# Performance work log

Measured on AMD Instinct MI355X. Metric: run time of the kernel, lower is better.

The kernel has to match this reference:

```python
import jax, jax.numpy as jnp
import numpy as np

V, E, U, B, S = 32000, 512, 1024, 16, 128
BN_EPS = 1e-3  # keras BatchNormalization default


def setup_inputs() -> dict:
    key = jax.random.key(0)
    ks = jax.random.split(key, 12)
    w = 0.05  # small init keeps the relu-activated LSTM recurrence stable
    return {
        "inputs": jax.random.randint(ks[0], (B, S), 0, V),
        "enc_hidden": jax.random.normal(ks[1], (B, U), jnp.float32) * 0.1,
        "enc_cell": jax.random.normal(ks[2], (B, U), jnp.float32) * 0.1,
        "emb": jax.random.normal(ks[3], (V, E), jnp.float32) * w,
        "Wx": jax.random.normal(ks[4], (E, 4 * U), jnp.float32) * w,
        "Wh": jax.random.normal(ks[5], (U, 4 * U), jnp.float32) * w,
        "b": jnp.zeros((4 * U,), jnp.float32),
        "gamma": jnp.ones((U,), jnp.float32),
        "beta": jnp.zeros((U,), jnp.float32),
        "mov_mean": jnp.zeros((U,), jnp.float32),
        "mov_var": jnp.ones((U,), jnp.float32),
        "W1": jax.random.normal(ks[6], (U, U), jnp.float32) * w,
        "b1": jnp.zeros((U,), jnp.float32),
        "W2": jax.random.normal(ks[7], (U, V), jnp.float32) * w,
        "b2": jnp.zeros((V,), jnp.float32),
    }


def _lstm_relu(xg, mask, h0, c0, Wh):
    # xg: [S,B,4U] precomputed input gates; mask: [S,B] (mask_zero semantics)
    def step(carry, inp):
        h, c = carry
        g, m = inp
        z = g + h @ Wh  # [B,4U]
        i, f, cc, o = jnp.split(z, 4, axis=-1)  # keras gate order i,f,c,o
        i = jax.nn.sigmoid(i)
        f = jax.nn.sigmoid(f)
        o = jax.nn.sigmoid(o)
        cc = jax.nn.relu(cc)  # activation='relu' on candidate
        c_new = f * c + i * cc
        h_new = o * jax.nn.relu(c_new)  # activation='relu' on output
        m = m[:, None]
        h_new = jnp.where(m, h_new, h)  # masked step: carry state/output
        c_new = jnp.where(m, c_new, c)
        return (h_new, c_new), h_new

    (_, _), hs = jax.lax.scan(step, (h0, c0), (xg, mask))
    return hs  # [S,B,U]


def reference(inputs, enc_hidden, enc_cell, emb, Wx, Wh, b, gamma, beta,
              mov_mean, mov_var, W1, b1, W2, b2):
    x = emb[inputs]                       # [B,S,E]
    mask = (inputs != 0)                  # mask_zero=True
    xg = jnp.einsum("bse,eg->bsg", x, Wx) + b   # [B,S,4U]
    hs = _lstm_relu(xg.transpose(1, 0, 2), mask.T, enc_hidden, enc_cell, Wh)
    h = hs.transpose(1, 0, 2)             # [B,S,U]
    # BatchNorm (inference: moving statistics), Dropout is identity at inference
    hbn = (h - mov_mean) * jax.lax.rsqrt(mov_var + BN_EPS) * gamma + beta
    d1 = jax.nn.relu(hbn @ W1 + b1)       # [B,S,U]
    logits = d1 @ W2 + b2                 # [B,S,V]
    return jax.nn.softmax(logits, axis=-1)
```

## Files before the change

kernel.cpp:

```cpp
#include <hip/hip_runtime.h>
#include <hip/hip_bf16.h>
#include <stdint.h>

typedef unsigned short u16;
typedef unsigned int u32;
typedef unsigned long long u64;
typedef __attribute__((ext_vector_type(4))) float f32x4;
typedef __attribute__((ext_vector_type(8))) short s16x8;
typedef __attribute__((ext_vector_type(4))) unsigned int u32x4;

#define AT_LD(p)    __hip_atomic_load((p), __ATOMIC_RELAXED, __HIP_MEMORY_SCOPE_AGENT)
#define AT_ST(p, v) __hip_atomic_store((p), (v), __ATOMIC_RELAXED, __HIP_MEMORY_SCOPE_AGENT)
#define AT_FAA(p)   __hip_atomic_fetch_add((p), 1u, __ATOMIC_RELAXED, __HIP_MEMORY_SCOPE_AGENT)


static __device__ __forceinline__ u16 f2bf(float f) {
  union { float f; unsigned u; } v; v.f = f;
  unsigned r = v.u + 0x7FFFu + ((v.u >> 16) & 1u);
  return (u16)(r >> 16);
}

static __device__ __forceinline__ float bf2f(u16 b) {
  union { unsigned u; float f; } v; v.u = ((u32)b) << 16;
  return v.f;
}

static __device__ __forceinline__ void gload_lds16(const void* g, void* l) {
  __builtin_amdgcn_global_load_lds(
      (const __attribute__((address_space(1))) unsigned int*)(uintptr_t)g,
      (__attribute__((address_space(3))) unsigned int*)(uintptr_t)l,
      16, 0, 0);
}

static __device__ __forceinline__ int swzB(int B) {
  int pos = (B >> 4) & 127;
  int row = (B >> 11) & 15;
  int slot = (pos ^ row ^ (pos >> 3)) & 7;
  int npos = (pos & 0x78) | slot;
  return (B & ~0x7F0) | (npos << 4);
}


__global__ void embed_kernel(const int* __restrict__ inputs,
                             const float* __restrict__ emb,
                             u16* __restrict__ xbf) {
  int i = blockIdx.x * 256 + threadIdx.x;
  int row = i >> 6;
  int e0 = (i & 63) << 3;
  int tok = inputs[row];
  const float* src = emb + (size_t)tok * 512 + e0;
  s16x8 o;
#pragma unroll
  for (int j = 0; j < 8; ++j) o[j] = (short)f2bf(src[j]);
  *(s16x8*)(xbf + (size_t)row * 512 + e0) = o;
}

__global__ void mask_kernel(const int* __restrict__ inputs, u64* __restrict__ mb) {
  int t = threadIdx.x;
  if (t < 32) {
    int b = t >> 1, h = t & 1;
    u64 m = 0;
    for (int j = 0; j < 64; ++j)
      m |= (u64)(inputs[b * 128 + h * 64 + j] != 0) << j;
    mb[t] = m;
  }
}

__global__ void transpose_bf16(const float* __restrict__ W, u16* __restrict__ Wt,
                               int K, int N) {
  __shared__ float t[32][33];
  int ntn = N >> 5;
  int tn = blockIdx.x % ntn, tk = blockIdx.x / ntn;
  int n0 = tn << 5, k0 = tk << 5;
  int tx = threadIdx.x & 31, ty = threadIdx.x >> 5;
#pragma unroll
  for (int j = 0; j < 4; ++j) {
    int k = ty * 4 + j;
    t[k][tx] = W[(size_t)(k0 + k) * N + n0 + tx];
  }
  __syncthreads();
#pragma unroll
  for (int j = 0; j < 4; ++j) {
    int n = ty * 4 + j;
    Wt[(size_t)(n0 + n) * K + k0 + tx] = f2bf(t[tx][n]);
  }
}

template <int MODE>
__global__ __launch_bounds__(256)
void gemm_bf16(const u16* __restrict__ A, const u16* __restrict__ Bt,
               const float* __restrict__ bias, void* __restrict__ Cptr,
               float* __restrict__ rowsum, int M, int N, int K) {
  (void)M;
  __shared__ u16 sA[128 * 32];
  __shared__ u16 sB[128 * 32];
  const int nbn = N >> 7;
  const int nwg = gridDim.x;
  int bid = blockIdx.x;
  int q = nwg >> 3;
  int swz = (bid & 7) * q + (bid >> 3);
  int bm = swz / nbn, bn = swz % nbn;
  const int brow = bm << 7, bcol = bn << 7;

  const int tid = threadIdx.x;
  const int lane = tid & 63;
  const int wv = tid >> 6;
  const int wr = (wv >> 1) * 64, wc = (wv & 1) * 64;
  const int ln = lane & 15, kh = lane >> 4;

  const int srow = tid >> 2;
  const int kch = (tid & 3) << 3;

  f32x4 acc[4][4] = {};

  const int nk = K >> 5;
  const u16* Abase = A + (size_t)(brow + srow) * K + kch;
  const u16* Bbase = Bt + (size_t)(bcol + srow) * K + kch;
  const size_t rstride = (size_t)64 * K;
  u16* lA = sA + srow * 32 + kch;
  u16* lB = sB + srow * 32 + kch;

  for (int kt = 0; kt < nk; ++kt) {
    const int k0 = kt << 5;
    gload_lds16(Abase + k0, lA);
    gload_lds16(Abase + rstride + k0, lA + 64 * 32);
    gload_lds16(Bbase + k0, lB);
    gload_lds16(Bbase + rstride + k0, lB + 64 * 32);
    __syncthreads();
    s16x8 aF[4], bF[4];
#pragma unroll
    for (int m = 0; m < 4; ++m)
      aF[m] = *(const s16x8*)(sA + (wr + m * 16 + ln) * 32 + kh * 8);
#pragma unroll
    for (int n = 0; n < 4; ++n)
      bF[n] = *(const s16x8*)(sB + (wc + n * 16 + ln) * 32 + kh * 8);
#pragma unroll
    for (int m = 0; m < 4; ++m)
#pragma unroll
      for (int n = 0; n < 4; ++n)
        acc[m][n] = __builtin_amdgcn_mfma_f32_16x16x32_bf16(aF[m], bF[n], acc[m][n], 0, 0, 0);
    __syncthreads();
  }

  const int browq = brow + wr;
  const int bcolq = bcol + wc;

  if (MODE == 1) {
    u16* O = (u16*)Cptr;
#pragma unroll
    for (int n = 0; n < 4; ++n) {
      int gcol = bcolq + n * 16 + ln;
      float bv = bias[gcol];
#pragma unroll
      for (int m = 0; m < 4; ++m)
#pragma unroll
        for (int r = 0; r < 4; ++r) {
          int grow = browq + m * 16 + kh * 4 + r;
          float v = fmaxf(acc[m][n][r] + bv, 0.f);
          O[(size_t)grow * N + gcol] = f2bf(v);
        }
    }
  } else {
    float* O = (float*)Cptr;
    float rs[4][4] = {};
#pragma unroll
    for (int n = 0; n < 4; ++n) {
      int gcol = bcolq + n * 16 + ln;
      float bv = bias[gcol];
#pragma unroll
      for (int m = 0; m < 4; ++m)
#pragma unroll
        for (int r = 0; r < 4; ++r) {
          int grow = browq + m * 16 + kh * 4 + r;
          float v = acc[m][n][r] + bv;
          if (MODE == 2) { v = __expf(v); rs[m][r] += v; }
          O[(size_t)grow * N + gcol] = v;
        }
    }
    if (MODE == 2) {
#pragma unroll
      for (int m = 0; m < 4; ++m)
#pragma unroll
        for (int r = 0; r < 4; ++r) {
          float v = rs[m][r];
          v += __shfl_xor(v, 1);
          v += __shfl_xor(v, 2);
          v += __shfl_xor(v, 4);
          v += __shfl_xor(v, 8);
          if (ln == 0) atomicAdd(&rowsum[browq + m * 16 + kh * 4 + r], v);
        }
    }
  }
}

__global__ __launch_bounds__(512, 1)
void gemm256_exp(const u16* __restrict__ A, const u16* __restrict__ Bt,
                 const float* __restrict__ bias, u16* __restrict__ O,
                 float* __restrict__ rowsum, int M, int N, int K) {
  (void)M;
  __shared__ char lds[131072];
  const int nbn = N >> 8;
  const int nwg = gridDim.x;
  int bid = blockIdx.x;
  int q = nwg >> 3;
  int swz = (bid & 7) * q + (bid >> 3);
  int bm = swz / nbn, bn = swz % nbn;
  const int brow = bm << 8, bcol = bn << 8;

  const int tid = threadIdx.x;
  const int lane = tid & 63;
  const int wv = tid >> 6;
  const int wm = wv >> 2, wn = wv & 3;
  const int ln = lane & 15, kh = lane >> 4;

  const int nk = K >> 5;

  const u16* sbase[4];
#pragma unroll
  for (int j = 0; j < 4; ++j) {
    int cc = (j & 1) * 512 + wv * 64 + lane;
    int row = cc >> 2, pcol = cc & 3;
    int lcol = pcol ^ ((row >> 1) & 3);
    sbase[j] = (j < 2 ? A + (size_t)(brow + row) * K
                      : Bt + (size_t)(bcol + row) * K) + lcol * 8;
  }

#define STAGE256(kt, buf)                                                  \
  {                                                                        \
    char* lb = lds + (buf) * 32768 + wv * 1024;                            \
    _Pragma("unroll")                                                      \
    for (int j = 0; j < 4; ++j)                                            \
      gload_lds16(sbase[j] + (kt) * 32, lb + j * 8192);                    \
  }

  f32x4 acc[8][4] = {};

  STAGE256(0, 0);
  STAGE256(1, 1);
  asm volatile("s_waitcnt vmcnt(4)" ::: "memory");
  __syncthreads();

  const char* Ab = lds + (size_t)(wm * 128) * 64;
  const char* Bb = lds + 16384 + (size_t)(wn * 64) * 64;
  const int cswz = (kh ^ ((ln >> 1) & 3)) * 16 + ln * 64;

  for (int t = 0; t < nk; ++t) {
    const int boff = (t & 3) * 32768;
    if (t + 2 < nk) STAGE256(t + 2, (t + 2) & 3);
    s16x8 aF[8], bF[4];
#pragma unroll
    for (int m = 0; m < 8; ++m)
      aF[m] = *(const s16x8*)(Ab + boff + m * 1024 + cswz);
#pragma unroll
    for (int n = 0; n < 4; ++n)
      bF[n] = *(const s16x8*)(Bb + boff + n * 1024 + cswz);
    __builtin_amdgcn_s_setprio(1);
#pragma unroll
    for (int m = 0; m < 8; ++m)
#pragma unroll
      for (int n = 0; n < 4; ++n)
        acc[m][n] = __builtin_amdgcn_mfma_f32_16x16x32_bf16(aF[m], bF[n], acc[m][n], 0, 0, 0);
    __builtin_amdgcn_s_setprio(0);
    if (t + 2 < nk)
      asm volatile("s_waitcnt vmcnt(4)" ::: "memory");
    else
      asm volatile("s_waitcnt vmcnt(0)" ::: "memory");
    if (t < nk - 1) __syncthreads();
  }

  const int browq = brow + wm * 128;
  const int bcolq = bcol + wn * 64;
  float rs[8][4] = {};
#pragma unroll
  for (int n = 0; n < 4; ++n) {
    int gcol = bcolq + n * 16 + ln;
    float bv = bias[gcol];
#pragma unroll
    for (int m = 0; m < 8; ++m)
#pragma unroll
      for (int r = 0; r < 4; ++r) {
        float v = __expf(acc[m][n][r] + bv);
        rs[m][r] += v;
        O[(size_t)(browq + m * 16 + kh * 4 + r) * N + gcol] = f2bf(v);
      }
  }
#pragma unroll
  for (int m = 0; m < 8; ++m)
#pragma unroll
    for (int r = 0; r < 4; ++r) {
      float v = rs[m][r];
      v += __shfl_xor(v, 1);
      v += __shfl_xor(v, 2);
      v += __shfl_xor(v, 4);
      v += __shfl_xor(v, 8);
      if (ln == 0) atomicAdd(&rowsum[browq + m * 16 + kh * 4 + r], v);
    }
#undef STAGE256
}

__global__ __attribute__((amdgpu_flat_work_group_size(512, 512), amdgpu_waves_per_eu(2, 2)))
void lstm_kernel(const float* __restrict__ xg,
                 const u16* __restrict__ Wht,
                 const u64* __restrict__ maskb,
                 const float* __restrict__ ench, const float* __restrict__ encc,
                 const float* __restrict__ gamma, const float* __restrict__ beta,
                 const float* __restrict__ mmean, const float* __restrict__ mvar,
                 u32* __restrict__ hbuf32,
                 u16* __restrict__ hbn,
                 u32* __restrict__ cnt) {
  __shared__ char hA[32 * 1024];

  const int wg = blockIdx.x;
  const int u0 = wg << 5;
  const int tid = threadIdx.x;
  const int lane = tid & 63;
  const int wv = tid >> 6;
  const int ln = lane & 15, khq = lane >> 4;

  const int g = ln & 3;
  const int unit = u0 + wv * 4 + (ln >> 2);

  u32 bA[128];
  {
    const u16* wrow = Wht + (size_t)(g * 1024 + unit) * 1024 + khq * 8;
#pragma unroll
    for (int gq = 0; gq < 4; ++gq) {
      u32x4 t[8];
#pragma unroll
      for (int j = 0; j < 8; ++j) {
        const u16* pp = wrow + (gq * 8 + j) * 32;
        asm volatile("global_load_dwordx4 %0, %1, off" : "=v"(t[j]) : "v"(pp));
      }
      asm volatile("s_waitcnt vmcnt(0)" ::: "memory");
      __builtin_amdgcn_sched_barrier(0);
#pragma unroll
      for (int j = 0; j < 8; ++j) {
        int base = (gq * 8 + j) * 4;
        asm volatile("v_accvgpr_write_b32 %0, %1" : "=a"(bA[base + 0]) : "v"(t[j].x));
        asm volatile("v_accvgpr_write_b32 %0, %1" : "=a"(bA[base + 1]) : "v"(t[j].y));
        asm volatile("v_accvgpr_write_b32 %0, %1" : "=a"(bA[base + 2]) : "v"(t[j].z));
        asm volatile("v_accvgpr_write_b32 %0, %1" : "=a"(bA[base + 3]) : "v"(t[j].w));
      }
    }
  }

  float cellR[4], holdR[4], xgr[4];
  u64 mA[4], mB[4];
  const float bn_s = gamma[unit] * rsqrtf(mvar[unit] + 1e-3f);
  const float bn_b = beta[unit] - mmean[unit] * bn_s;
  const size_t bstride = (size_t)128 * 4096;
  const float* xbase = xg + (size_t)(khq * 4) * bstride + g * 1024 + unit;
#pragma unroll
  for (int r = 0; r < 4; ++r) {
    int batch = khq * 4 + r;
    cellR[r] = encc[batch * 1024 + unit];
    holdR[r] = ench[batch * 1024 + unit];
    mA[r] = maskb[batch * 2];
    mB[r] = maskb[batch * 2 + 1];
  }
#pragma unroll
  for (int r = 0; r < 4; ++r) {
    u32 w = (u32)f2bf(holdR[r]);
    u32 pw = (u32)__shfl_xor((int)w, 4);
    if ((ln & 7) == 0) {
      int batch = khq * 4 + r;
      AT_ST((u32*)((char*)hbuf32 + batch * 2048 + unit * 2), (w & 0xFFFFu) | (pw << 16));
    }
  }
#pragma unroll
  for (int r = 0; r < 4; ++r) xgr[r] = xbase[r * bstride];
  asm volatile("s_waitcnt vmcnt(0)" ::: "memory");
  __syncthreads();
  if (tid == 0) {
    u32 oldv = AT_FAA(cnt);
    if (oldv != 31u) {
      int c = 0;
      while (AT_LD((const u32*)cnt) < 32u) {
        __builtin_amdgcn_s_sleep(1);
        if (++c > (1 << 18)) break;
      }
    }
  }
  __syncthreads();

  for (int s = 0; s < 128; ++s) {
    u64 st[8];
    {
      const u64* base = (const u64*)((const char*)hbuf32 + (s & 1) * 32768) + tid;
#pragma unroll
      for (int k = 0; k < 8; ++k) {
        const u64* pp = base + k * 512;
        asm volatile("global_load_dwordx2 %0, %1, off sc0 sc1" : "=v"(st[k]) : "v"(pp));
      }
      asm volatile("s_waitcnt vmcnt(0)" ::: "memory");
      __builtin_amdgcn_sched_barrier(0);
#pragma unroll
      for (int k = 0; k < 8; ++k)
        *(u64*)(hA + swzB((tid + k * 512) * 8)) = st[k];
    }
    __syncthreads();

    f32x4 acc0 = {0.f, 0.f, 0.f, 0.f};
    f32x4 acc1 = {0.f, 0.f, 0.f, 0.f};
#pragma unroll
    for (int kt = 0; kt < 32; kt += 2) {
      s16x8 a0 = *(const s16x8*)(hA + swzB(ln * 2048 + kt * 64 + khq * 16));
      u32 w0, w1, w2, w3;
      asm("v_accvgpr_read_b32 %0, %1" : "=v"(w0) : "a"(bA[4 * kt + 0]));
      asm("v_accvgpr_read_b32 %0, %1" : "=v"(w1) : "a"(bA[4 * kt + 1]));
      asm("v_accvgpr_read_b32 %0, %1" : "=v"(w2) : "a"(bA[4 * kt + 2]));
      asm("v_accvgpr_read_b32 %0, %1" : "=v"(w3) : "a"(bA[4 * kt + 3]));
      u32x4 q0 = {w0, w1, w2, w3};
      acc0 = __builtin_amdgcn_mfma_f32_16x16x32_bf16(
          a0, __builtin_bit_cast(s16x8, q0), acc0, 0, 0, 0);
      s16x8 a1 = *(const s16x8*)(hA + swzB(ln * 2048 + (kt + 1) * 64 + khq * 16));
      u32 y0, y1, y2, y3;
      asm("v_accvgpr_read_b32 %0, %1" : "=v"(y0) : "a"(bA[4 * kt + 4]));
      asm("v_accvgpr_read_b32 %0, %1" : "=v"(y1) : "a"(bA[4 * kt + 5]));
      asm("v_accvgpr_read_b32 %0, %1" : "=v"(y2) : "a"(bA[4 * kt + 6]));
      asm("v_accvgpr_read_b32 %0, %1" : "=v"(y3) : "a"(bA[4 * kt + 7]));
      u32x4 q1 = {y0, y1, y2, y3};
      acc1 = __builtin_amdgcn_mfma_f32_16x16x32_bf16(
          a1, __builtin_bit_cast(s16x8, q1), acc1, 0, 0, 0);
    }
    f32x4 accs = acc0 + acc1;

    u32 bnpair[4];
    {
      u16 hbb[4], hbnb[4];
#pragma unroll
      for (int r = 0; r < 4; ++r) {
        float z = accs[r] + xgr[r];
        float sig = 1.f / (1.f + __expf(-z));
        float val = (g == 2) ? fmaxf(z, 0.f) : sig;
        float v1 = __shfl_xor(val, 1);
        float v2 = __shfl_xor(val, 2);
        float v3 = __shfl_xor(val, 3);
        float cnew = v1 * cellR[r] + val * v2;
        float hnew = v3 * fmaxf(cnew, 0.f);
        u64 mm = (s < 64) ? mA[r] : mB[r];
        if (!((mm >> (s & 63)) & 1)) { cnew = cellR[r]; hnew = holdR[r]; }
        cellR[r] = cnew;
        holdR[r] = hnew;
        hbb[r] = f2bf(hnew);
        hbnb[r] = f2bf(hnew * bn_s + bn_b);
      }
#pragma unroll
      for (int r = 0; r < 4; ++r) {
        u32 w = (u32)hbb[r] | ((u32)hbnb[r] << 16);
        u32 pw = (u32)__shfl_xor((int)w, 4);
        u32 hpair = (w & 0xFFFFu) | ((pw & 0xFFFFu) << 16);
        bnpair[r] = (w >> 16) | (pw & 0xFFFF0000u);
        if (s < 127 && (ln & 7) == 0) {
          int batch = khq * 4 + r;
          AT_ST((u32*)((char*)hbuf32 + ((s + 1) & 1) * 32768 + batch * 2048 + unit * 2), hpair);
        }
      }
    }

    if (s < 127) {
      asm volatile("s_waitcnt vmcnt(0)" ::: "memory");
      __syncthreads();
      u32 oldv = 0xFFFFFFFFu;
      if (tid == 0) oldv = AT_FAA(cnt);
      if ((ln & 7) == 0) {
#pragma unroll
        for (int r = 0; r < 4; ++r) {
          int batch = khq * 4 + r;
          *(u32*)((char*)hbn + (size_t)(batch * 128 + s) * 2048 + unit * 2) = bnpair[r];
        }
      }
      {
        const float* xb = xbase + (size_t)(s + 1) * 4096;
#pragma unroll
        for (int r = 0; r < 4; ++r) xgr[r] = xb[r * bstride];
      }
      if (tid == 0) {
        const u32 target = (u32)(s + 2) * 32u;
        if (oldv != target - 1u) {
          int c = 0;
          while (AT_LD((const u32*)cnt) < target) {
            __builtin_amdgcn_s_sleep(1);
            if (++c > (1 << 18)) break;
          }
        }
      }
      __syncthreads();
    } else if ((ln & 7) == 0) {
#pragma unroll
      for (int r = 0; r < 4; ++r) {
        int batch = khq * 4 + r;
        *(u32*)((char*)hbn + (size_t)(batch * 128 + s) * 2048 + unit * 2) = bnpair[r];
      }
    }
  }
}


__global__ void scale_kernel(float* __restrict__ out, const float* __restrict__ rs) {
  const int total4 = 16384000;
  for (int i = blockIdx.x * 256 + threadIdx.x; i < total4; i += gridDim.x * 256) {
    float4* p = (float4*)out + i;
    float4 v = *p;
    int row = i / 8000;
    float sF = 1.0f / rs[row];
    v.x *= sF; v.y *= sF; v.z *= sF; v.w *= sF;
    *p = v;
  }
}

__global__ void scale_bf_kernel(float* __restrict__ out, const u16* __restrict__ e,
                                const float* __restrict__ rs) {
  const int total8 = 8192000;
  for (int i = blockIdx.x * 256 + threadIdx.x; i < total8; i += gridDim.x * 256) {
    s16x8 v = ((const s16x8*)e)[i];
    int row = i / 4000;
    float sF = 1.0f / rs[row];
    float4 o0, o1;
    o0.x = bf2f((u16)v[0]) * sF; o0.y = bf2f((u16)v[1]) * sF;
    o0.z = bf2f((u16)v[2]) * sF; o0.w = bf2f((u16)v[3]) * sF;
    o1.x = bf2f((u16)v[4]) * sF; o1.y = bf2f((u16)v[5]) * sF;
    o1.z = bf2f((u16)v[6]) * sF; o1.w = bf2f((u16)v[7]) * sF;
    ((float4*)out)[2 * i] = o0;
    ((float4*)out)[2 * i + 1] = o1;
  }
}


extern "C" void kernel_launch(void* const* d_in, const int* in_sizes, int n_in,
                              void* d_out, int out_size, void* d_ws, size_t ws_size,
                              hipStream_t stream) {
  (void)in_sizes; (void)n_in; (void)out_size;
  const int*   inputs = (const int*)d_in[0];
  const float* ench   = (const float*)d_in[1];
  const float* encc   = (const float*)d_in[2];
  const float* emb    = (const float*)d_in[3];
  const float* Wx     = (const float*)d_in[4];
  const float* Wh     = (const float*)d_in[5];
  const float* bb     = (const float*)d_in[6];
  const float* gamma  = (const float*)d_in[7];
  const float* beta   = (const float*)d_in[8];
  const float* mmean  = (const float*)d_in[9];
  const float* mvar   = (const float*)d_in[10];
  const float* W1     = (const float*)d_in[11];
  const float* b1     = (const float*)d_in[12];
  const float* W2     = (const float*)d_in[13];
  const float* b2     = (const float*)d_in[14];
  float* out = (float*)d_out;

  char* p = (char*)d_ws;
  u32*   cnt    = (u32*)(p + 0);
  float* rowsum = (float*)(p + 1024);
  u64*   maskb  = (u64*)(p + 10240);
  u32*   hbuf32 = (u32*)(p + 16384);
  size_t off = 81920;
  u16*   xbf  = (u16*)(p + off);     off += (size_t)2048 * 512 * 2;
  u16*   Wxt  = (u16*)(p + off);     off += (size_t)4096 * 512 * 2;
  u16*   Wht  = (u16*)(p + off);     off += (size_t)4096 * 1024 * 2;
  u16*   W1t  = (u16*)(p + off);     off += (size_t)1024 * 1024 * 2;
  u16*   W2t  = (u16*)(p + off);     off += (size_t)32000 * 1024 * 2;
  float* xg   = (float*)(p + off);   off += (size_t)2048 * 4096 * 4;
  u16*   hbn  = (u16*)(p + off);     off += (size_t)2048 * 1024 * 2;
  u16*   d1   = (u16*)(p + off);     off += (size_t)2048 * 1024 * 2;
  size_t off_base = off;
  u16*   expbf = (u16*)(p + off);    off += (size_t)2048 * 32000 * 2;
  if (ws_size < off_base) return;
  const bool bf16path = (ws_size >= off);

  hipMemsetAsync(d_ws, 0, 9216, stream);

  embed_kernel<<<512, 256, 0, stream>>>(inputs, emb, xbf);
  mask_kernel<<<1, 64, 0, stream>>>(inputs, maskb);
  transpose_bf16<<<(512 / 32) * (4096 / 32), 256, 0, stream>>>(Wx, Wxt, 512, 4096);
  transpose_bf16<<<(1024 / 32) * (4096 / 32), 256, 0, stream>>>(Wh, Wht, 1024, 4096);
  transpose_bf16<<<(1024 / 32) * (1024 / 32), 256, 0, stream>>>(W1, W1t, 1024, 1024);
  transpose_bf16<<<(1024 / 32) * (32000 / 32), 256, 0, stream>>>(W2, W2t, 1024, 32000);

  gemm_bf16<0><<<16 * 32, 256, 0, stream>>>(xbf, Wxt, bb, xg, nullptr, 2048, 4096, 512);

  lstm_kernel<<<32, 512, 0, stream>>>(xg, Wht, maskb, ench, encc, gamma, beta,
                                      mmean, mvar, hbuf32, hbn, cnt);

  gemm_bf16<1><<<16 * 8, 256, 0, stream>>>(hbn, W1t, b1, d1, nullptr, 2048, 1024, 1024);

  if (bf16path) {
    gemm256_exp<<<8 * 125, 512, 0, stream>>>(d1, W2t, b2, expbf, rowsum, 2048, 32000, 1024);
    scale_bf_kernel<<<2048, 256, 0, stream>>>(out, expbf, rowsum);
  } else {
    gemm_bf16<2><<<16 * 250, 256, 0, stream>>>(d1, W2t, b2, out, rowsum, 2048, 32000, 1024);
    scale_kernel<<<2048, 256, 0, stream>>>(out, rowsum);
  }
}
```

Baseline: 912.9 us.

## Split LSTM recurrent matmul over K across waves with LDS partial-sum reduction

Each wave previously staged the whole hidden state into LDS and ran the full K=1024 MFMA chain for its own 16 gate columns. Now each wave covers a quarter of K for 64 gate columns, loading its A fragments straight from global into registers, which drops the LDS staging copy and the swizzle. Partial accumulators go to a small LDS buffer and are summed after one barrier. The aim is to cut per-step global-to-LDS traffic and shorten the serial MFMA dependency chain, at the cost of a cross-wave reduction and four independent accumulators.

```diff
diff --git a/kernel.cpp b/kernel.cpp
--- a/kernel.cpp
+++ b/kernel.cpp
@@ -30,14 +30,6 @@
       (const __attribute__((address_space(1))) unsigned int*)(uintptr_t)g,
       (__attribute__((address_space(3))) unsigned int*)(uintptr_t)l,
       16, 0, 0);
-}
-
-static __device__ __forceinline__ int swzB(int B) {
-  int pos = (B >> 4) & 127;
-  int row = (B >> 11) & 15;
-  int slot = (pos ^ row ^ (pos >> 3)) & 7;
-  int npos = (pos & 0x78) | slot;
-  return (B & ~0x7F0) | (npos << 4);
 }
 
 
@@ -308,7 +300,7 @@
                  u32* __restrict__ hbuf32,
                  u16* __restrict__ hbn,
                  u32* __restrict__ cnt) {
-  __shared__ char hA[32 * 1024];
+  __shared__ f32x4 zxP[8][16][16];
 
   const int wg = blockIdx.x;
   const int u0 = wg << 5;
@@ -316,19 +308,22 @@
   const int lane = tid & 63;
   const int wv = tid >> 6;
   const int ln = lane & 15, khq = lane >> 4;
+  const int ks = wv >> 1, ng = wv & 1;
 
   const int g = ln & 3;
   const int unit = u0 + wv * 4 + (ln >> 2);
 
   u32 bA[128];
   {
-    const u16* wrow = Wht + (size_t)(g * 1024 + unit) * 1024 + khq * 8;
 #pragma unroll
     for (int gq = 0; gq < 4; ++gq) {
       u32x4 t[8];
 #pragma unroll
       for (int j = 0; j < 8; ++j) {
-        const u16* pp = wrow + (gq * 8 + j) * 32;
+        int qi = gq * 8 + j;
+        int nf = qi >> 3, kt = qi & 7;
+        const u16* pp = Wht + (size_t)(g * 1024 + u0 + ng * 16 + nf * 4 + (ln >> 2)) * 1024
+                        + ks * 256 + kt * 32 + khq * 8;
         asm volatile("global_load_dwordx4 %0, %1, off" : "=v"(t[j]) : "v"(pp));
       }
       asm volatile("s_waitcnt vmcnt(0)" ::: "memory");
@@ -384,53 +379,53 @@
   __syncthreads();
 
   for (int s = 0; s < 128; ++s) {
-    u64 st[8];
+    u32x4 aQ[8];
     {
-      const u64* base = (const u64*)((const char*)hbuf32 + (s & 1) * 32768) + tid;
-#pragma unroll
-      for (int k = 0; k < 8; ++k) {
-        const u64* pp = base + k * 512;
-        asm volatile("global_load_dwordx2 %0, %1, off sc0 sc1" : "=v"(st[k]) : "v"(pp));
+      const char* abase = (const char*)hbuf32 + (s & 1) * 32768 +
+                          ln * 2048 + ks * 512 + khq * 16;
+#pragma unroll
+      for (int kt = 0; kt < 8; ++kt) {
+        const char* pp = abase + kt * 64;
+        asm volatile("global_load_dwordx4 %0, %1, off sc0 sc1" : "=v"(aQ[kt]) : "v"(pp));
       }
       asm volatile("s_waitcnt vmcnt(0)" ::: "memory");
       __builtin_amdgcn_sched_barrier(0);
-#pragma unroll
-      for (int k = 0; k < 8; ++k)
-        *(u64*)(hA + swzB((tid + k * 512) * 8)) = st[k];
-    }
+    }
+
+    f32x4 acc[4] = {};
+#pragma unroll
+    for (int kt = 0; kt < 8; ++kt) {
+      s16x8 a = __builtin_bit_cast(s16x8, aQ[kt]);
+#pragma unroll
+      for (int nf = 0; nf < 4; ++nf) {
+        int qi = (nf * 8 + kt) * 4;
+        u32 w0, w1, w2, w3;
+        asm("v_accvgpr_read_b32 %0, %1" : "=v"(w0) : "a"(bA[qi + 0]));
+        asm("v_accvgpr_read_b32 %0, %1" : "=v"(w1) : "a"(bA[qi + 1]));
+        asm("v_accvgpr_read_b32 %0, %1" : "=v"(w2) : "a"(bA[qi + 2]));
+        asm("v_accvgpr_read_b32 %0, %1" : "=v"(w3) : "a"(bA[qi + 3]));
+        u32x4 qv = {w0, w1, w2, w3};
+        acc[nf] = __builtin_amdgcn_mfma_f32_16x16x32_bf16(
+            a, __builtin_bit_cast(s16x8, qv), acc[nf], 0, 0, 0);
+      }
+    }
+
+#pragma unroll
+    for (int nf = 0; nf < 4; ++nf)
+      zxP[ng * 4 + nf][ln][(ks * 4 + khq) ^ ln] = acc[nf];
     __syncthreads();
 
-    f32x4 acc0 = {0.f, 0.f, 0.f, 0.f};
-    f32x4 acc1 = {0.f, 0.f, 0.f, 0.f};
-#pragma unroll
-    for (int kt = 0; kt < 32; kt += 2) {
-      s16x8 a0 = *(const s16x8*)(hA + swzB(ln * 2048 + kt * 64 + khq * 16));
-      u32 w0, w1, w2, w3;
-      asm("v_accvgpr_read_b32 %0, %1" : "=v"(w0) : "a"(bA[4 * kt + 0]));
-      asm("v_accvgpr_read_b32 %0, %1" : "=v"(w1) : "a"(bA[4 * kt + 1]));
-      asm("v_accvgpr_read_b32 %0, %1" : "=v"(w2) : "a"(bA[4 * kt + 2]));
-      asm("v_accvgpr_read_b32 %0, %1" : "=v"(w3) : "a"(bA[4 * kt + 3]));
-      u32x4 q0 = {w0, w1, w2, w3};
-      acc0 = __builtin_amdgcn_mfma_f32_16x16x32_bf16(
-          a0, __builtin_bit_cast(s16x8, q0), acc0, 0, 0, 0);
-      s16x8 a1 = *(const s16x8*)(hA + swzB(ln * 2048 + (kt + 1) * 64 + khq * 16));
-      u32 y0, y1, y2, y3;
-      asm("v_accvgpr_read_b32 %0, %1" : "=v"(y0) : "a"(bA[4 * kt + 4]));
-      asm("v_accvgpr_read_b32 %0, %1" : "=v"(y1) : "a"(bA[4 * kt + 5]));
-      asm("v_accvgpr_read_b32 %0, %1" : "=v"(y2) : "a"(bA[4 * kt + 6]));
-      asm("v_accvgpr_read_b32 %0, %1" : "=v"(y3) : "a"(bA[4 * kt + 7]));
-      u32x4 q1 = {y0, y1, y2, y3};
-      acc1 = __builtin_amdgcn_mfma_f32_16x16x32_bf16(
-          a1, __builtin_bit_cast(s16x8, q1), acc1, 0, 0, 0);
-    }
-    f32x4 accs = acc0 + acc1;
+    f32x4 zv = {0.f, 0.f, 0.f, 0.f};
+#pragma unroll
+    for (int k2 = 0; k2 < 4; ++k2)
+      zv += zxP[wv][ln][(k2 * 4 + khq) ^ ln];
 
     u32 bnpair[4];
     {
       u16 hbb[4], hbnb[4];
 #pragma unroll
       for (int r = 0; r < 4; ++r) {
-        float z = accs[r] + xgr[r];
+        float z = zv[r] + xgr[r];
         float sig = 1.f / (1.f + __expf(-z));
         float val = (g == 2) ? fmaxf(z, 0.f) : sig;
         float v1 = __shfl_xor(val, 1);
```

New measurement: 1.012 ms. 10.8% more time.
